# Kernel tuning notes

Measured on AMD Instinct MI355X. Metric: run time of the kernel, lower is better.

Reference implementation:

```python
import jax, jax.numpy as jnp
import numpy as np

N = 50000
HID = 128


def care_layer(h, src, dst, att_w, att_b, n_nodes):
    # att([x_i, x_j]) == x_i @ W[:H] + x_j @ W[H:]  (avoids materializing concat)
    H = h.shape[1]
    wi, wj = att_w[:H], att_w[H:]
    hi = h[dst]                                   # [E, H] gather (x_i = target)
    hj = h[src]                                   # [E, H] gather (x_j = source)
    alpha = jax.nn.sigmoid(hi @ wi + hj @ wj + att_b)  # [E, 1]
    msg = alpha * hj                              # [E, H]
    sums = jax.ops.segment_sum(msg, dst, num_segments=n_nodes)
    cnts = jax.ops.segment_sum(jnp.ones((src.shape[0],), h.dtype), dst, num_segments=n_nodes)
    return sums / jnp.maximum(cnts, 1.0)[:, None]  # scatter-mean; isolated nodes -> 0


def setup_inputs() -> dict:
    key = jax.random.key(0)
    ks = jax.random.split(key, 8)
    in_dim, hid, out_dim = 256, HID, 2
    x = jax.random.normal(ks[0], (N, in_dim), dtype=jnp.float32)
    edge_index = jax.random.randint(ks[1], (2, 1600000), 0, N, dtype=jnp.int64)
    s = lambda k, shp, fan: jax.random.normal(k, shp, jnp.float32) * (1.0 / np.sqrt(fan))
    return {
        "x": x,
        "edge_index": edge_index,
        "enc_w": s(ks[2], (in_dim, hid), in_dim),
        "enc_b": jnp.zeros((hid,), jnp.float32),
        "att1_w": s(ks[3], (2 * hid, 1), 2 * hid),
        "att1_b": jnp.zeros((1,), jnp.float32),
        "att2_w": s(ks[4], (2 * hid, 1), 2 * hid),
        "att2_b": jnp.zeros((1,), jnp.float32),
        "cls_w": s(ks[5], (hid, out_dim), hid),
        "cls_b": jnp.zeros((out_dim,), jnp.float32),
    }


def reference(x, edge_index, enc_w, enc_b, att1_w, att1_b, att2_w, att2_b, cls_w, cls_b):
    src, dst = edge_index[0], edge_index[1]  # PyG: x_j = x[src], aggregate at dst
    n = x.shape[0]
    h = jax.nn.relu(x @ enc_w + enc_b)       # dropout is identity in eval mode
    h = care_layer(h, src, dst, att1_w, att1_b, n)
    h = jax.nn.relu(h)
    h = care_layer(h, src, dst, att2_w, att2_b, n)
    return h @ cls_w + cls_b                 # [N, out_dim]
```

## Files before the change

### kernel.cpp

```cpp
#include <hip/hip_runtime.h>
#include <hip/hip_bf16.h>
#include <hip/hip_fp16.h>
#include <math.h>

#define HID 128
#define INDIM 256
#define CAP 2560
#define NBLK1 256

typedef _Float16 h2v __attribute__((ext_vector_type(2)));

#ifndef __has_builtin
#define __has_builtin(x) 0
#endif
#if __has_builtin(__builtin_amdgcn_fdot2)
#define FDOT2(a, b, c) __builtin_amdgcn_fdot2((a), (b), (c), false)
#else
__device__ __forceinline__ float FDOT2(h2v a, h2v b, float c) {
    return fmaf((float)a[0], (float)b[0], fmaf((float)a[1], (float)b[1], c));
}
#endif

__global__ void detect_i64_kernel(const int* __restrict__ idx32, int* __restrict__ flag) {
    int l = threadIdx.x;
    int v = idx32[2 * l + 1];
    unsigned long long ball = __ballot(v != 0);
    if (l == 0) flag[0] = (ball == 0ULL) ? 1 : 0;
}

__device__ __forceinline__ int load_src(const int* idx, int is64, int E, int e) {
    return is64 ? idx[2 * e] : idx[e];
}
__device__ __forceinline__ int load_dst(const int* idx, int is64, int E, int e) {
    return is64 ? idx[2 * (E + e)] : idx[E + e];
}

__global__ __launch_bounds__(256) void enc_scatter_kernel(
        const float* __restrict__ x, const float* __restrict__ W,
        const float* __restrict__ b, const float* __restrict__ attw,
        const float* __restrict__ attb, __half* __restrict__ h16,
        float* __restrict__ ai, float* __restrict__ aj, int N, int EBenc,
        const int* __restrict__ idx32, const int* __restrict__ flag,
        int* __restrict__ bcursor, unsigned int* __restrict__ recs, int E, int NB) {
    __shared__ __align__(16) char smem[12800];
    int t = threadIdx.x;

    if ((int)blockIdx.x >= EBenc) {
        int* hist = (int*)smem;
        int* cur  = (int*)(smem + 4096);
        int sbid = blockIdx.x - EBenc;
        int CH = (E + NBLK1 - 1) / NBLK1;
        int e0 = sbid * CH;
        int e1 = min(e0 + CH, E);
        for (int i = t; i < NB; i += 256) hist[i] = 0;
        __syncthreads();
        int is64 = flag[0];
        for (int e = e0 + t; e < e1; e += 256) {
            int d = load_dst(idx32, is64, E, e);
            atomicAdd(&hist[d >> 6], 1);
        }
        __syncthreads();
        for (int i = t; i < NB; i += 256)
            cur[i] = hist[i] ? atomicAdd(&bcursor[i], hist[i]) : 0;
        __syncthreads();
        for (int e = e0 + t; e < e1; e += 256) {
            int s = load_src(idx32, is64, E, e);
            int d = load_dst(idx32, is64, E, e);
            int bb = d >> 6;
            int r = atomicAdd(&cur[bb], 1);
            if (r < CAP)
                recs[(size_t)bb * CAP + r] = ((unsigned)d << 16) | (unsigned)s;
        }
        return;
    }

    h2v (*xsp)[68]  = (h2v(*)[68])smem;
    h2v (*wspT)[132] = (h2v(*)[132])(smem + 4352);
    int n0 = blockIdx.x * 64;
    int tc = t & 15, tr = t >> 4;
    int c0 = tc * 8, r0 = tr * 4;
    float acc[4][8];
    #pragma unroll
    for (int i = 0; i < 4; i++)
        #pragma unroll
        for (int j = 0; j < 8; j++) acc[i][j] = 0.f;

    int lr = t >> 2, lc4 = (t & 3) * 8;
    int wcg = t & 15, wk2 = t >> 4;

    for (int k0 = 0; k0 < INDIM; k0 += 32) {
        int gr = n0 + lr; if (gr >= N) gr = N - 1;
        const float4* xg = (const float4*)(x + (size_t)gr * INDIM + k0 + lc4);
        float4 a0 = xg[0], a1 = xg[1];
        int kb = lc4 >> 1;
        { h2v p; p[0] = (_Float16)a0.x; p[1] = (_Float16)a0.y; xsp[kb + 0][lr] = p; }
        { h2v p; p[0] = (_Float16)a0.z; p[1] = (_Float16)a0.w; xsp[kb + 1][lr] = p; }
        { h2v p; p[0] = (_Float16)a1.x; p[1] = (_Float16)a1.y; xsp[kb + 2][lr] = p; }
        { h2v p; p[0] = (_Float16)a1.z; p[1] = (_Float16)a1.w; xsp[kb + 3][lr] = p; }
        {
            const float4* w0 = (const float4*)(W + (size_t)(k0 + 2 * wk2) * HID + wcg * 8);
            const float4* w1 = (const float4*)(W + (size_t)(k0 + 2 * wk2 + 1) * HID + wcg * 8);
            float4 r0a = w0[0], r0b = w0[1];
            float4 r1a = w1[0], r1b = w1[1];
            union { float4 f; h2v h[4]; } ua, ub;
            ua.h[0][0] = (_Float16)r0a.x; ua.h[0][1] = (_Float16)r1a.x;
            ua.h[1][0] = (_Float16)r0a.y; ua.h[1][1] = (_Float16)r1a.y;
            ua.h[2][0] = (_Float16)r0a.z; ua.h[2][1] = (_Float16)r1a.z;
            ua.h[3][0] = (_Float16)r0a.w; ua.h[3][1] = (_Float16)r1a.w;
            ub.h[0][0] = (_Float16)r0b.x; ub.h[0][1] = (_Float16)r1b.x;
            ub.h[1][0] = (_Float16)r0b.y; ub.h[1][1] = (_Float16)r1b.y;
            ub.h[2][0] = (_Float16)r0b.z; ub.h[2][1] = (_Float16)r1b.z;
            ub.h[3][0] = (_Float16)r0b.w; ub.h[3][1] = (_Float16)r1b.w;
            *(float4*)&wspT[wcg][wk2 * 8]     = ua.f;
            *(float4*)&wspT[wcg][wk2 * 8 + 4] = ub.f;
        }
        __syncthreads();
        #pragma unroll
        for (int kk2 = 0; kk2 < 16; ++kk2) {
            union { float4 f; h2v h[4]; } ux, uw0, uw1;
            ux.f  = *(const float4*)&xsp[kk2][r0];
            uw0.f = *(const float4*)&wspT[tc][kk2 * 8];
            uw1.f = *(const float4*)&wspT[tc][kk2 * 8 + 4];
            #pragma unroll
            for (int i = 0; i < 4; i++) {
                #pragma unroll
                for (int j = 0; j < 4; j++) {
                    acc[i][j]     = FDOT2(ux.h[i], uw0.h[j], acc[i][j]);
                    acc[i][j + 4] = FDOT2(ux.h[i], uw1.h[j], acc[i][j + 4]);
                }
            }
        }
        __syncthreads();
    }
    float wiv[8], wjv[8];
    #pragma unroll
    for (int j = 0; j < 8; j++) { wiv[j] = attw[c0 + j]; wjv[j] = attw[HID + c0 + j]; }
    #pragma unroll
    for (int i = 0; i < 4; i++) {
        int gr = n0 + r0 + i;
        float ov[8];
        #pragma unroll
        for (int j = 0; j < 8; j++) {
            float o = acc[i][j] + b[c0 + j];
            ov[j] = o > 0.f ? o : 0.f;
        }
        if (gr < N) {
            union { float4 f; __half2 h[4]; } u;
            #pragma unroll
            for (int j = 0; j < 8; j += 2)
                u.h[j >> 1] = __float22half2_rn(make_float2(ov[j], ov[j + 1]));
            *(float4*)(h16 + (size_t)gr * HID + c0) = u.f;
        }
        float pi = 0.f, pj = 0.f;
        #pragma unroll
        for (int j = 0; j < 8; j++) { pi = fmaf(ov[j], wiv[j], pi); pj = fmaf(ov[j], wjv[j], pj); }
        #pragma unroll
        for (int off = 1; off < 16; off <<= 1) {
            pi += __shfl_xor(pi, off);
            pj += __shfl_xor(pj, off);
        }
        if (tc == 0 && gr < N) { ai[gr] = pi + attb[0]; aj[gr] = pj; }
    }
}

__global__ __launch_bounds__(256) void csr_finalize_kernel(const unsigned int* __restrict__ recs,
                                                           const int* __restrict__ bcursor,
                                                           int* __restrict__ rowstart,
                                                           int* __restrict__ csr_src,
                                                           int N, int E) {
    __shared__ int h[64];
    __shared__ int ex[64];
    __shared__ int cu[64];
    __shared__ int wred[4];
    int b = blockIdx.x;
    int t = threadIdx.x;
    int lane = t & 63, w = t >> 6;
    int partial = 0;
    for (int i = t; i < b; i += 256) partial += bcursor[i];
    #pragma unroll
    for (int off = 32; off >= 1; off >>= 1) partial += __shfl_xor(partial, off);
    if (lane == 0) wred[w] = partial;
    if (t < 64) h[t] = 0;
    __syncthreads();
    int base = wred[0] + wred[1] + wred[2] + wred[3];
    int cnt = bcursor[b]; if (cnt > CAP) cnt = CAP;
    const unsigned int* r0 = recs + (size_t)b * CAP;
    for (int i = t; i < cnt; i += 256) {
        unsigned int rec = r0[i];
        atomicAdd(&h[(rec >> 16) & 63], 1);
    }
    __syncthreads();
    if (w == 0) {
        int s = h[lane];
        int x = s;
        #pragma unroll
        for (int off = 1; off < 64; off <<= 1) {
            int y = __shfl_up(x, off);
            if (lane >= off) x += y;
        }
        ex[lane] = x - s;
    }
    __syncthreads();
    int d0 = b * 64;
    if (t < 64) {
        if (d0 + t < N) rowstart[d0 + t] = base + ex[t];
        cu[t] = ex[t];
    }
    if (b == 0 && t == 0) rowstart[N] = E;
    __syncthreads();
    for (int i = t; i < cnt; i += 256) {
        unsigned int rec = r0[i];
        int dl = (rec >> 16) & 63;
        int r = atomicAdd(&cu[dl], 1);
        csr_src[base + r] = (int)(rec & 0xffffu);
    }
}

template <int MODE>
__global__ __launch_bounds__(256) void care_kernel(const __half* __restrict__ hh,
                                                   const float* __restrict__ ai,
                                                   const float* __restrict__ aj,
                                                   const int* __restrict__ rowstart,
                                                   const int* __restrict__ csr_src,
                                                   float* __restrict__ out,
                                                   __half* __restrict__ hh_out,
                                                   float* __restrict__ ai2,
                                                   float* __restrict__ aj2, int N,
                                                   const float* __restrict__ attw2,
                                                   const float* __restrict__ attb2,
                                                   const float* __restrict__ clsw,
                                                   const float* __restrict__ clsb) {
    int t = threadIdx.x;
    int lane = t & 63, w = t >> 6;
    int n = blockIdx.x * 4 + w;
    if (n >= N) return;
    int beg = rowstart[n], end = rowstart[n + 1];
    int deg = end - beg;
    float ain = ai[n];
    int g = lane >> 4;
    int r = lane & 15;

    float acc[8];
    #pragma unroll
    for (int k = 0; k < 8; k++) acc[k] = 0.f;

    const float4* hp = (const float4*)hh;
    for (int c0 = beg; c0 < end; c0 += 64) {
        int m = end - c0; if (m > 64) m = 64;
        int li = lane < m ? lane : m - 1;
        int sl = csr_src[c0 + li];
        float ajl = aj[sl];
        float al = 1.0f / (1.0f + __expf(-(ain + ajl)));
        if (lane >= m) al = 0.f;
        int nit = (m + 3) >> 2;
        #pragma unroll 4
        for (int it = 0; it < nit; ++it) {
            int idx = it * 4 + g;
            float a = __shfl(al, idx);
            int s = __shfl(sl, idx);
            float4 hv = hp[(size_t)s * 16 + r];
            union { float4 f; __half2 h[4]; } u; u.f = hv;
            #pragma unroll
            for (int k = 0; k < 4; k++) {
                float2 fv = __half22float2(u.h[k]);
                acc[2 * k + 0] = fmaf(a, fv.x, acc[2 * k + 0]);
                acc[2 * k + 1] = fmaf(a, fv.y, acc[2 * k + 1]);
            }
        }
    }
    #pragma unroll
    for (int k = 0; k < 8; k++) {
        acc[k] += __shfl_xor(acc[k], 16);
        acc[k] += __shfl_xor(acc[k], 32);
    }
    float scale = 1.0f / fmaxf((float)deg, 1.0f);

    if (MODE == 0) {
        float mv[8];
        #pragma unroll
        for (int k = 0; k < 8; k++) {
            float o = acc[k] * scale;
            mv[k] = o > 0.f ? o : 0.f;
        }
        if (g == 0) {
            union { float4 f; __half2 h[4]; } u;
            #pragma unroll
            for (int k = 0; k < 4; k++)
                u.h[k] = __float22half2_rn(make_float2(mv[2 * k], mv[2 * k + 1]));
            ((float4*)hh_out)[(size_t)n * 16 + r] = u.f;
        }
        float pi = 0.f, pj = 0.f;
        #pragma unroll
        for (int k = 0; k < 8; k++) {
            int f = r * 8 + k;
            pi = fmaf(mv[k], attw2[f], pi);
            pj = fmaf(mv[k], attw2[HID + f], pj);
        }
        #pragma unroll
        for (int off = 1; off < 16; off <<= 1) {
            pi += __shfl_xor(pi, off);
            pj += __shfl_xor(pj, off);
        }
        if (lane == 0) { ai2[n] = pi + attb2[0]; aj2[n] = pj; }
    } else {
        float p0 = 0.f, p1 = 0.f;
        #pragma unroll
        for (int k = 0; k < 8; k++) {
            float m = acc[k] * scale;
            int f = r * 8 + k;
            p0 = fmaf(m, clsw[f * 2 + 0], p0);
            p1 = fmaf(m, clsw[f * 2 + 1], p1);
        }
        #pragma unroll
        for (int off = 8; off >= 1; off >>= 1) {
            p0 += __shfl_xor(p0, off);
            p1 += __shfl_xor(p1, off);
        }
        if (lane == 0) {
            out[(size_t)n * 2 + 0] = p0 + clsb[0];
            out[(size_t)n * 2 + 1] = p1 + clsb[1];
        }
    }
}

extern "C" void kernel_launch(void* const* d_in, const int* in_sizes, int n_in,
                              void* d_out, int out_size, void* d_ws, size_t ws_size,
                              hipStream_t stream) {
    const float* x      = (const float*)d_in[0];
    const int*   idx32  = (const int*)d_in[1];
    const float* enc_w  = (const float*)d_in[2];
    const float* enc_b  = (const float*)d_in[3];
    const float* att1_w = (const float*)d_in[4];
    const float* att1_b = (const float*)d_in[5];
    const float* att2_w = (const float*)d_in[6];
    const float* att2_b = (const float*)d_in[7];
    const float* cls_w  = (const float*)d_in[8];
    const float* cls_b  = (const float*)d_in[9];
    float* out = (float*)d_out;

    int N = in_sizes[0] / INDIM;
    int E = in_sizes[1] / 2;
    int NB = (N + 63) >> 6;
    int EBenc = (N + 63) / 64;

    char* p = (char*)d_ws;
    __half* h16a = (__half*)p; p += (size_t)N * HID * 2;
    __half* h16b = (__half*)p; p += (size_t)N * HID * 2;
    int* csr_src  = (int*)p; p += (size_t)E * 4;
    unsigned int* recs = (unsigned int*)p; p += (size_t)NB * CAP * 4;
    float* ai   = (float*)p; p += (size_t)N * 4;
    float* aj   = (float*)p; p += (size_t)N * 4;
    float* ai2  = (float*)p; p += (size_t)N * 4;
    float* aj2  = (float*)p; p += (size_t)N * 4;
    int* rowstart = (int*)p; p += (size_t)(N + 1) * 4;
    int* bcursor  = (int*)p; p += (size_t)NB * 4;
    int* flag     = (int*)p; p += 64;

    hipMemsetAsync(bcursor, 0, (size_t)NB * 4, stream);
    detect_i64_kernel<<<1, 64, 0, stream>>>(idx32, flag);
    enc_scatter_kernel<<<EBenc + NBLK1, 256, 0, stream>>>(x, enc_w, enc_b, att1_w, att1_b,
                                                          h16a, ai, aj, N, EBenc,
                                                          idx32, flag, bcursor, recs, E, NB);
    csr_finalize_kernel<<<NB, 256, 0, stream>>>(recs, bcursor, rowstart, csr_src, N, E);

    care_kernel<0><<<(N + 3) / 4, 256, 0, stream>>>(h16a, ai, aj, rowstart, csr_src,
                                                    nullptr, h16b, ai2, aj2, N,
                                                    att2_w, att2_b, nullptr, nullptr);
    care_kernel<1><<<(N + 3) / 4, 256, 0, stream>>>(h16b, ai2, aj2, rowstart, csr_src,
                                                    out, nullptr, nullptr, nullptr, N,
                                                    nullptr, nullptr, cls_w, cls_b);
}
```

Baseline: 272.7 us.

## Fuse CSR finalize with first CARE layer using LDS-resident bucket sources

Merges the CSR finalize kernel with the first aggregation layer. Each 512-thread block builds the CSR for its 64-node bucket, keeps the source list in shared memory, and immediately aggregates those nodes. This removes one launch and a global re-read of csr_src and rowstart for layer one. It also raises NBLK1 in the scatter kernel. In exchange the fused kernel runs only NB blocks with a large LDS footprint, which may limit occupancy and latency hiding for the gather-heavy aggregation.

Result: no change. 269.8 us (-1.1%).

```diff
diff --git a/kernel.cpp b/kernel.cpp
--- a/kernel.cpp
+++ b/kernel.cpp
@@ -6,7 +6,7 @@
 #define HID 128
 #define INDIM 256
 #define CAP 2560
-#define NBLK1 256
+#define NBLK1 512
 
 typedef _Float16 h2v __attribute__((ext_vector_type(2)));
 
@@ -163,73 +163,144 @@
     }
 }
 
-__global__ __launch_bounds__(256) void csr_finalize_kernel(const unsigned int* __restrict__ recs,
-                                                           const int* __restrict__ bcursor,
-                                                           int* __restrict__ rowstart,
-                                                           int* __restrict__ csr_src,
-                                                           int N, int E) {
+__global__ __launch_bounds__(512) void care_bucket0_kernel(
+        const __half* __restrict__ hh, const float* __restrict__ ai,
+        const float* __restrict__ aj, const int* __restrict__ bcursor,
+        const unsigned int* __restrict__ recs,
+        int* __restrict__ rowstart, int* __restrict__ csr_src,
+        __half* __restrict__ hh_out, float* __restrict__ ai2,
+        float* __restrict__ aj2, int N, int E,
+        const float* __restrict__ attw2, const float* __restrict__ attb2) {
+    __shared__ int lsrc[CAP];
     __shared__ int h[64];
     __shared__ int ex[64];
     __shared__ int cu[64];
-    __shared__ int wred[4];
+    __shared__ float ail[64];
+    __shared__ int wred[8];
     int b = blockIdx.x;
     int t = threadIdx.x;
     int lane = t & 63, w = t >> 6;
+    int d0 = b * 64;
+
     int partial = 0;
-    for (int i = t; i < b; i += 256) partial += bcursor[i];
+    for (int i = t; i < b; i += 512) partial += bcursor[i];
     #pragma unroll
     for (int off = 32; off >= 1; off >>= 1) partial += __shfl_xor(partial, off);
     if (lane == 0) wred[w] = partial;
-    if (t < 64) h[t] = 0;
+    if (t < 64) { h[t] = 0; ail[t] = (d0 + t < N) ? ai[d0 + t] : 0.f; }
     __syncthreads();
-    int base = wred[0] + wred[1] + wred[2] + wred[3];
+    int base = 0;
+    #pragma unroll
+    for (int k = 0; k < 8; k++) base += wred[k];
     int cnt = bcursor[b]; if (cnt > CAP) cnt = CAP;
     const unsigned int* r0 = recs + (size_t)b * CAP;
-    for (int i = t; i < cnt; i += 256) {
-        unsigned int rec = r0[i];
-        atomicAdd(&h[(rec >> 16) & 63], 1);
-    }
+
+    for (int i = t; i < cnt; i += 512)
+        atomicAdd(&h[(r0[i] >> 16) & 63], 1);
     __syncthreads();
     if (w == 0) {
         int s = h[lane];
-        int x = s;
+        int xx = s;
         #pragma unroll
         for (int off = 1; off < 64; off <<= 1) {
-            int y = __shfl_up(x, off);
-            if (lane >= off) x += y;
-        }
-        ex[lane] = x - s;
+            int y = __shfl_up(xx, off);
+            if (lane >= off) xx += y;
+        }
+        ex[lane] = xx - s;
     }
     __syncthreads();
-    int d0 = b * 64;
     if (t < 64) {
         if (d0 + t < N) rowstart[d0 + t] = base + ex[t];
         cu[t] = ex[t];
     }
     if (b == 0 && t == 0) rowstart[N] = E;
     __syncthreads();
-    for (int i = t; i < cnt; i += 256) {
+    for (int i = t; i < cnt; i += 512) {
         unsigned int rec = r0[i];
         int dl = (rec >> 16) & 63;
+        int s = (int)(rec & 0xffffu);
         int r = atomicAdd(&cu[dl], 1);
-        csr_src[base + r] = (int)(rec & 0xffffu);
-    }
-}
-
-template <int MODE>
-__global__ __launch_bounds__(256) void care_kernel(const __half* __restrict__ hh,
-                                                   const float* __restrict__ ai,
-                                                   const float* __restrict__ aj,
-                                                   const int* __restrict__ rowstart,
-                                                   const int* __restrict__ csr_src,
-                                                   float* __restrict__ out,
-                                                   __half* __restrict__ hh_out,
-                                                   float* __restrict__ ai2,
-                                                   float* __restrict__ aj2, int N,
-                                                   const float* __restrict__ attw2,
-                                                   const float* __restrict__ attb2,
-                                                   const float* __restrict__ clsw,
-                                                   const float* __restrict__ clsb) {
+        lsrc[r] = s;
+        csr_src[base + r] = s;
+    }
+    __syncthreads();
+
+    const float4* hp = (const float4*)hh;
+    int g = lane >> 4, r = lane & 15;
+    for (int ds = w; ds < 64; ds += 8) {
+        int n = d0 + ds;
+        if (n >= N) continue;
+        int beg = ex[ds], deg = h[ds];
+        float ain = ail[ds];
+        float acc[8];
+        #pragma unroll
+        for (int k = 0; k < 8; k++) acc[k] = 0.f;
+        for (int c0 = beg; c0 < beg + deg; c0 += 64) {
+            int m = beg + deg - c0; if (m > 64) m = 64;
+            int li = lane < m ? lane : m - 1;
+            int sl = lsrc[c0 + li];
+            float ajl = aj[sl];
+            float al = 1.0f / (1.0f + __expf(-(ain + ajl)));
+            if (lane >= m) al = 0.f;
+            int nit = (m + 3) >> 2;
+            #pragma unroll 4
+            for (int it = 0; it < nit; ++it) {
+                int idx = it * 4 + g;
+                float a = __shfl(al, idx);
+                int s = __shfl(sl, idx);
+                float4 hv = hp[(size_t)s * 16 + r];
+                union { float4 f; __half2 hx[4]; } u; u.f = hv;
+                #pragma unroll
+                for (int k = 0; k < 4; k++) {
+                    float2 fv = __half22float2(u.hx[k]);
+                    acc[2 * k + 0] = fmaf(a, fv.x, acc[2 * k + 0]);
+                    acc[2 * k + 1] = fmaf(a, fv.y, acc[2 * k + 1]);
+                }
+            }
+        }
+        #pragma unroll
+        for (int k = 0; k < 8; k++) {
+            acc[k] += __shfl_xor(acc[k], 16);
+            acc[k] += __shfl_xor(acc[k], 32);
+        }
+        float scale = 1.0f / fmaxf((float)deg, 1.0f);
+        float mv[8];
+        #pragma unroll
+        for (int k = 0; k < 8; k++) {
+            float o = acc[k] * scale;
+            mv[k] = o > 0.f ? o : 0.f;
+        }
+        if (g == 0) {
+            union { float4 f; __half2 hx[4]; } u;
+            #pragma unroll
+            for (int k = 0; k < 4; k++)
+                u.hx[k] = __float22half2_rn(make_float2(mv[2 * k], mv[2 * k + 1]));
+            ((float4*)hh_out)[(size_t)n * 16 + r] = u.f;
+        }
+        float pi = 0.f, pj = 0.f;
+        #pragma unroll
+        for (int k = 0; k < 8; k++) {
+            int f = r * 8 + k;
+            pi = fmaf(mv[k], attw2[f], pi);
+            pj = fmaf(mv[k], attw2[HID + f], pj);
+        }
+        #pragma unroll
+        for (int off = 1; off < 16; off <<= 1) {
+            pi += __shfl_xor(pi, off);
+            pj += __shfl_xor(pj, off);
+        }
+        if (lane == 0) { ai2[n] = pi + attb2[0]; aj2[n] = pj; }
+    }
+}
+
+__global__ __launch_bounds__(256) void care_kernel1(const __half* __restrict__ hh,
+                                                    const float* __restrict__ ai,
+                                                    const float* __restrict__ aj,
+                                                    const int* __restrict__ rowstart,
+                                                    const int* __restrict__ csr_src,
+                                                    float* __restrict__ out, int N,
+                                                    const float* __restrict__ clsw,
+                                                    const float* __restrict__ clsb) {
     int t = threadIdx.x;
     int lane = t & 63, w = t >> 6;
     int n = blockIdx.x * 4 + w;
@@ -259,10 +330,10 @@
             float a = __shfl(al, idx);
             int s = __shfl(sl, idx);
             float4 hv = hp[(size_t)s * 16 + r];
-            union { float4 f; __half2 h[4]; } u; u.f = hv;
+            union { float4 f; __half2 hx[4]; } u; u.f = hv;
             #pragma unroll
             for (int k = 0; k < 4; k++) {
-                float2 fv = __half22float2(u.h[k]);
+                float2 fv = __half22float2(u.hx[k]);
                 acc[2 * k + 0] = fmaf(a, fv.x, acc[2 * k + 0]);
                 acc[2 * k + 1] = fmaf(a, fv.y, acc[2 * k + 1]);
             }
@@ -274,52 +345,22 @@
         acc[k] += __shfl_xor(acc[k], 32);
     }
     float scale = 1.0f / fmaxf((float)deg, 1.0f);
-
-    if (MODE == 0) {
-        float mv[8];
-        #pragma unroll
-        for (int k = 0; k < 8; k++) {
-            float o = acc[k] * scale;
-            mv[k] = o > 0.f ? o : 0.f;
-        }
-        if (g == 0) {
-            union { float4 f; __half2 h[4]; } u;
-            #pragma unroll
-            for (int k = 0; k < 4; k++)
-                u.h[k] = __float22half2_rn(make_float2(mv[2 * k], mv[2 * k + 1]));
-            ((float4*)hh_out)[(size_t)n * 16 + r] = u.f;
-        }
-        float pi = 0.f, pj = 0.f;
-        #pragma unroll
-        for (int k = 0; k < 8; k++) {
-            int f = r * 8 + k;
-            pi = fmaf(mv[k], attw2[f], pi);
-            pj = fmaf(mv[k], attw2[HID + f], pj);
-        }
-        #pragma unroll
-        for (int off = 1; off < 16; off <<= 1) {
-            pi += __shfl_xor(pi, off);
-            pj += __shfl_xor(pj, off);
-        }
-        if (lane == 0) { ai2[n] = pi + attb2[0]; aj2[n] = pj; }
-    } else {
-        float p0 = 0.f, p1 = 0.f;
-        #pragma unroll
-        for (int k = 0; k < 8; k++) {
-            float m = acc[k] * scale;
-            int f = r * 8 + k;
-            p0 = fmaf(m, clsw[f * 2 + 0], p0);
-            p1 = fmaf(m, clsw[f * 2 + 1], p1);
-        }
-        #pragma unroll
-        for (int off = 8; off >= 1; off >>= 1) {
-            p0 += __shfl_xor(p0, off);
-            p1 += __shfl_xor(p1, off);
-        }
-        if (lane == 0) {
-            out[(size_t)n * 2 + 0] = p0 + clsb[0];
-            out[(size_t)n * 2 + 1] = p1 + clsb[1];
-        }
+    float p0 = 0.f, p1 = 0.f;
+    #pragma unroll
+    for (int k = 0; k < 8; k++) {
+        float m = acc[k] * scale;
+        int f = r * 8 + k;
+        p0 = fmaf(m, clsw[f * 2 + 0], p0);
+        p1 = fmaf(m, clsw[f * 2 + 1], p1);
+    }
+    #pragma unroll
+    for (int off = 8; off >= 1; off >>= 1) {
+        p0 += __shfl_xor(p0, off);
+        p1 += __shfl_xor(p1, off);
+    }
+    if (lane == 0) {
+        out[(size_t)n * 2 + 0] = p0 + clsb[0];
+        out[(size_t)n * 2 + 1] = p1 + clsb[1];
     }
 }
 
@@ -361,12 +402,9 @@
     enc_scatter_kernel<<<EBenc + NBLK1, 256, 0, stream>>>(x, enc_w, enc_b, att1_w, att1_b,
                                                           h16a, ai, aj, N, EBenc,
                                                           idx32, flag, bcursor, recs, E, NB);
-    csr_finalize_kernel<<<NB, 256, 0, stream>>>(recs, bcursor, rowstart, csr_src, N, E);
-
-    care_kernel<0><<<(N + 3) / 4, 256, 0, stream>>>(h16a, ai, aj, rowstart, csr_src,
-                                                    nullptr, h16b, ai2, aj2, N,
-                                                    att2_w, att2_b, nullptr, nullptr);
-    care_kernel<1><<<(N + 3) / 4, 256, 0, stream>>>(h16b, ai2, aj2, rowstart, csr_src,
-                                                    out, nullptr, nullptr, nullptr, N,
-                                                    nullptr, nullptr, cls_w, cls_b);
-}
+    care_bucket0_kernel<<<NB, 512, 0, stream>>>(h16a, ai, aj, bcursor, recs,
+                                                rowstart, csr_src, h16b, ai2, aj2,
+                                                N, E, att2_w, att2_b);
+    care_kernel1<<<(N + 3) / 4, 256, 0, stream>>>(h16b, ai2, aj2, rowstart, csr_src,
+                                                  out, N, cls_w, cls_b);
+}
```
